# Performance work log

Measured on AMD Instinct MI355X. Metric: run time of the kernel, lower is better.

The kernel has to match this reference:

```python
import jax, jax.numpy as jnp
import numpy as np

B, S, M, D, H, F, E, K = 4, 1024, 1024, 1024, 16, 4096, 4, 2
DH = D // H
LB_COEF = 0.01
LN_EPS = 1e-5


def setup_inputs() -> dict:
    key = jax.random.key(0)
    ks = jax.random.split(key, 16)
    w = lambda k, shape: jax.random.normal(k, shape, jnp.float32) * 0.02
    return {
        "x": jax.random.normal(ks[0], (B, S, D), jnp.float32),
        "memory": jax.random.normal(ks[1], (B, M, D), jnp.float32),
        "sWq": w(ks[2], (D, D)), "sWk": w(ks[3], (D, D)),
        "sWv": w(ks[4], (D, D)), "sWo": w(ks[5], (D, D)),
        "cWq": w(ks[6], (D, D)), "cWk": w(ks[7], (D, D)),
        "cWv": w(ks[8], (D, D)), "cWo": w(ks[9], (D, D)),
        "Wg": w(ks[10], (E, D)),
        "W1": w(ks[11], (E, F, D)), "b1": jnp.zeros((E, F), jnp.float32),
        "W2": w(ks[12], (E, D, F)), "b2": jnp.zeros((E, D), jnp.float32),
        "ln1_g": jnp.ones((D,), jnp.float32), "ln1_b": jnp.zeros((D,), jnp.float32),
        "ln2_g": jnp.ones((D,), jnp.float32), "ln2_b": jnp.zeros((D,), jnp.float32),
        "ln3_g": jnp.ones((D,), jnp.float32), "ln3_b": jnp.zeros((D,), jnp.float32),
    }


def _ln(x, g, b):
    m = x.mean(-1, keepdims=True)
    v = ((x - m) ** 2).mean(-1, keepdims=True)
    return (x - m) * jax.lax.rsqrt(v + LN_EPS) * g + b


def _mha(q_in, k_in, v_in, Wq, Wk, Wv, Wo):
    # nn.Linear(bias=False): y = x @ W.T; split into heads [b, h, s, dh]
    def split(t):
        b, s, _ = t.shape
        return t.reshape(b, s, H, DH).transpose(0, 2, 1, 3)
    Q = split(q_in @ Wq.T)
    Kh = split(k_in @ Wk.T)
    V = split(v_in @ Wv.T)
    scores = jnp.einsum('bhqd,bhkd->bhqk', Q, Kh) / jnp.sqrt(jnp.float32(DH))
    attn = jax.nn.softmax(scores, axis=-1)  # dropout is identity in eval
    out = jnp.einsum('bhqk,bhkd->bhqd', attn, V)
    b, _, s, _ = out.shape
    out = out.transpose(0, 2, 1, 3).reshape(b, s, D)
    return out @ Wo.T


def _moe(h, Wg, W1, b1, W2, b2):
    gate_logits = h @ Wg.T                      # [B, S, E]
    gate_probs = jax.nn.softmax(gate_logits, -1)
    topk_logits, topk_idx = jax.lax.top_k(gate_logits, K)
    topk_w = jax.nn.softmax(topk_logits, -1)    # [B, S, K]
    # dense all-experts FFN (faithful to source): [B, S, E, F] hidden
    hid = jax.nn.gelu(jnp.einsum('bsd,efd->bsef', h, W1) + b1, approximate=False)
    eo = jnp.einsum('bsef,edf->bsed', hid, W2) + b2   # [B, S, E, D]
    sel = jnp.take_along_axis(eo, topk_idx[..., None], axis=2)  # [B, S, K, D]
    out = (sel * topk_w[..., None]).sum(axis=2)
    one_hot = jax.nn.one_hot(topk_idx, E, dtype=gate_probs.dtype)  # [B, S, K, E]
    load = one_hot.sum(axis=2).mean(axis=(0, 1))   # [E]
    imp = gate_probs.mean(axis=(0, 1))             # [E]
    aux = LB_COEF * (E * jnp.sum(load * imp))
    return out, aux


def reference(x, memory, sWq, sWk, sWv, sWo, cWq, cWk, cWv, cWo,
              Wg, W1, b1, W2, b2,
              ln1_g, ln1_b, ln2_g, ln2_b, ln3_g, ln3_b):
    h = _ln(x, ln1_g, ln1_b)
    x = x + _mha(h, h, h, sWq, sWk, sWv, sWo)
    h = _ln(x, ln2_g, ln2_b)
    x = x + _mha(h, memory, memory, cWq, cWk, cWv, cWo)
    h = _ln(x, ln3_g, ln3_b)
    ffn_out, aux = _moe(h, Wg, W1, b1, W2, b2)
    return (x + ffn_out, aux)
```

## Files before the change

kernel.cpp:

```cpp
#include <hip/hip_runtime.h>
#include <math.h>
#include <stdint.h>

typedef unsigned short u16;
typedef _Float16 f16;
typedef __attribute__((ext_vector_type(8))) _Float16 f16x8;
typedef __attribute__((ext_vector_type(8))) short s16x8;
typedef __attribute__((ext_vector_type(4))) float f32x4;
typedef __attribute__((ext_vector_type(4))) unsigned short u16x4;

#define DEV static __device__ __forceinline__

#define MFMA16(a, b, c) __builtin_amdgcn_mfma_f32_16x16x32_f16((a), (b), (c), 0, 0, 0)

DEV void split2(float v, u16& hi, u16& lo) {
  f16 h = (f16)v;
  f16 l = (f16)(v - (float)h);
  hi = __builtin_bit_cast(u16, h);
  lo = __builtin_bit_cast(u16, l);
}
DEV u16 f2h(float v) { f16 h = (f16)v; return __builtin_bit_cast(u16, h); }
DEV float h2f(u16 u) { f16 h = __builtin_bit_cast(f16, u); return (float)h; }

DEV void gload16(const void* gp, const void* lp) {
  typedef const __attribute__((address_space(1))) unsigned GU;
  typedef __attribute__((address_space(3))) unsigned LU;
  GU* g = (GU*)(uintptr_t)gp;
  LU* l = (LU*)(unsigned)(uintptr_t)lp;
  __builtin_amdgcn_global_load_lds(g, l, 16, 0, 0);
}

DEV int swzP(int q) { return ((q & 3) << 4) ^ (((q >> 2) & 3) << 5); }

enum { EPI3_SPLIT = 0, EPI3_RESID = 1 };

template <int EPI>
__global__ __launch_bounds__(256, 2)
void gemm3(const u16* __restrict__ Ah, const u16* __restrict__ Al,
           const u16* __restrict__ Bh, const u16* __restrict__ Bl,
           int N, int K, int ldC,
           u16* __restrict__ outh, u16* __restrict__ outl,
           float* __restrict__ outf, const float* __restrict__ resid)
{
  __shared__ alignas(16) u16 sAh[128 * 32], sAl[128 * 32];
  __shared__ alignas(16) u16 sBh[128 * 32], sBl[128 * 32];
  const int tid = threadIdx.x;
  const int wave = tid >> 6, lane = tid & 63;
  const int wr = wave >> 1, wc = wave & 1;
  const int li = lane & 15, g = lane >> 4;
  const long row0 = (long)blockIdx.y * 128;
  const int col0 = blockIdx.x * 128;

  const int srow = lane >> 2;
  const int scol = (lane & 3) * 8;
  const long arow = (row0 + wave * 32 + srow) * (long)K + scol;
  const long brow = ((long)col0 + wave * 32 + srow) * (long)K + scol;
  const u16 *gAh = Ah + arow, *gAl = Al + arow;
  const u16 *gBh = Bh + brow, *gBl = Bl + brow;
  u16 *lAh = sAh + wave * 1024, *lAl = sAl + wave * 1024;
  u16 *lBh = sBh + wave * 1024, *lBl = sBl + wave * 1024;

  const f32x4 fz = {0.f, 0.f, 0.f, 0.f};
  f32x4 acc[4][4];
#pragma unroll
  for (int m = 0; m < 4; m++)
#pragma unroll
    for (int n = 0; n < 4; n++) acc[m][n] = fz;

  const int aoff = (wr * 64 + li) * 32 + g * 8;
  const int boff = (wc * 64 + li) * 32 + g * 8;

  for (int k0 = 0; k0 < K; k0 += 32) {
    gload16(gAh + k0, lAh); gload16(gAh + k0 + (long)16 * K, lAh + 512);
    gload16(gAl + k0, lAl); gload16(gAl + k0 + (long)16 * K, lAl + 512);
    gload16(gBh + k0, lBh); gload16(gBh + k0 + (long)16 * K, lBh + 512);
    gload16(gBl + k0, lBl); gload16(gBl + k0 + (long)16 * K, lBl + 512);
    __syncthreads();
    f16x8 ah[4], al4[4], bh[4], bl4[4];
#pragma unroll
    for (int m = 0; m < 4; m++) {
      ah[m] = *(const f16x8*)(sAh + aoff + m * 512);
      al4[m] = *(const f16x8*)(sAl + aoff + m * 512);
    }
#pragma unroll
    for (int n = 0; n < 4; n++) {
      bh[n] = *(const f16x8*)(sBh + boff + n * 512);
      bl4[n] = *(const f16x8*)(sBl + boff + n * 512);
    }
#pragma unroll
    for (int m = 0; m < 4; m++)
#pragma unroll
      for (int n = 0; n < 4; n++) {
        f32x4 t = acc[m][n];
        t = MFMA16(al4[m], bh[n], t);
        t = MFMA16(ah[m], bl4[n], t);
        t = MFMA16(ah[m], bh[n], t);
        acc[m][n] = t;
      }
    __syncthreads();
  }

#pragma unroll
  for (int m = 0; m < 4; m++)
#pragma unroll
    for (int n = 0; n < 4; n++) {
      const int col = col0 + wc * 64 + n * 16 + li;
#pragma unroll
      for (int r = 0; r < 4; r++) {
        const long row = row0 + wr * 64 + m * 16 + g * 4 + r;
        const long idx = row * ldC + col;
        const float v = acc[m][n][r];
        if constexpr (EPI == EPI3_SPLIT) {
          u16 hi, lo; split2(v, hi, lo);
          outh[idx] = hi; outl[idx] = lo;
        } else {
          outf[idx] = resid[idx] + v;
        }
      }
    }
}

__global__ __launch_bounds__(256)
void vtrans(const u16* __restrict__ Vh, const u16* __restrict__ Vl,
            u16* __restrict__ Th, u16* __restrict__ Tl)
{
  __shared__ u16 t0[64][80];
  __shared__ u16 t1[64][80];
  const int kb = blockIdx.x, h = blockIdx.y, b = blockIdx.z;
  const int tid = threadIdx.x;
  const int r = tid >> 2;
  const int c = tid & 3;
  const long srow = ((long)b * 1024 + kb * 64 + r) * 3072 + h * 64;
  s16x8 a0 = *(const s16x8*)(Vh + srow + c * 8);
  s16x8 a1 = *(const s16x8*)(Vh + srow + c * 8 + 32);
  s16x8 b0 = *(const s16x8*)(Vl + srow + c * 8);
  s16x8 b1 = *(const s16x8*)(Vl + srow + c * 8 + 32);
#pragma unroll
  for (int j = 0; j < 8; j++) {
    t0[c * 8 + j][r]      = (u16)(short)a0[j];
    t0[c * 8 + 32 + j][r] = (u16)(short)a1[j];
    t1[c * 8 + j][r]      = (u16)(short)b0[j];
    t1[c * 8 + 32 + j][r] = (u16)(short)b1[j];
  }
  __syncthreads();
  const int dh = tid >> 2;
  const long drow = ((long)(b * 16 + h) * 64 + dh) * 1024 + kb * 64;
  s16x8 o0, o1;
#pragma unroll
  for (int j = 0; j < 8; j++) {
    o0[j] = (short)t0[dh][c * 8 + j];
    o1[j] = (short)t0[dh][c * 8 + 32 + j];
  }
  *(s16x8*)(Th + drow + c * 8) = o0;
  *(s16x8*)(Th + drow + c * 8 + 32) = o1;
#pragma unroll
  for (int j = 0; j < 8; j++) {
    o0[j] = (short)t1[dh][c * 8 + j];
    o1[j] = (short)t1[dh][c * 8 + 32 + j];
  }
  *(s16x8*)(Tl + drow + c * 8) = o0;
  *(s16x8*)(Tl + drow + c * 8 + 32) = o1;
}

__global__ __launch_bounds__(512, 4)
void attn3(const u16* __restrict__ Qh, const u16* __restrict__ Ql,
           const u16* __restrict__ Kbh, const u16* __restrict__ Kbl,
           const u16* __restrict__ Vth, const u16* __restrict__ Vtl,
           u16* __restrict__ AOh, u16* __restrict__ AOl)
{
  __shared__ alignas(16) u16 lKh[64 * 64], lKl[64 * 64];
  __shared__ alignas(16) u16 lVh[64 * 64], lVl[64 * 64];
  __shared__ alignas(16) u16 lPh[8 * 16 * 64], lPl[8 * 16 * 64];
  const int tid = threadIdx.x;
  const int wave = tid >> 6, lane = tid & 63;
  const int li = lane & 15, g = lane >> 4;
  const int qt = blockIdx.x, h = blockIdx.y, b = blockIdx.z;
  const int bh = b * 16 + h;
  const int LD = 3072;

  const long qrow0 = (long)b * 1024 + qt * 128 + wave * 16;
  f16x8 qfh[2], qfl[2];
#pragma unroll
  for (int kk = 0; kk < 2; kk++) {
    const long qoff = (qrow0 + li) * LD + h * 64 + kk * 32 + g * 8;
    qfh[kk] = *(const f16x8*)(Qh + qoff);
    qfl[kk] = *(const f16x8*)(Ql + qoff);
  }

  const f32x4 fz = {0.f, 0.f, 0.f, 0.f};
  float m_run[4], l_run[4];
  f32x4 oacc[4];
#pragma unroll
  for (int r = 0; r < 4; r++) { m_run[r] = -INFINITY; l_run[r] = 0.f; }
#pragma unroll
  for (int d = 0; d < 4; d++) oacc[d] = fz;

  char* cKh = (char*)lKh; char* cKl = (char*)lKl;
  char* cVh = (char*)lVh; char* cVl = (char*)lVl;
  char* cPh = (char*)lPh + wave * 2048;
  char* cPl = (char*)lPl + wave * 2048;

  const int kr = tid >> 3;
  const int kce = (tid & 7) * 8;
  const u16* kbase_h = Kbh + ((long)b * 1024 + kr) * LD + h * 64 + kce;
  const u16* kbase_l = Kbl + ((long)b * 1024 + kr) * LD + h * 64 + kce;
  const u16* vbase_h = Vth + ((long)bh * 64 + kr) * 1024 + kce;
  const u16* vbase_l = Vtl + ((long)bh * 64 + kr) * 1024 + kce;
  const int sdst = kr * 128 + ((kce * 2) ^ ((kr & 7) << 4));

  s16x8 rkh, rkl, rvh, rvl;
#define LOADT(t)                                                   \
  {                                                                \
    const long ko = (long)(t) * 64 * LD;                           \
    const int vo = (t) * 64;                                       \
    rkh = *(const s16x8*)(kbase_h + ko);                           \
    rkl = *(const s16x8*)(kbase_l + ko);                           \
    rvh = *(const s16x8*)(vbase_h + vo);                           \
    rvl = *(const s16x8*)(vbase_l + vo);                           \
  }

  LOADT(0);

  for (int t = 0; t < 16; ++t) {
    __syncthreads();
    *(s16x8*)(cKh + sdst) = rkh;
    *(s16x8*)(cKl + sdst) = rkl;
    *(s16x8*)(cVh + sdst) = rvh;
    *(s16x8*)(cVl + sdst) = rvl;
    if (t < 15) LOADT(t + 1);
    __syncthreads();

    f32x4 s[4];
#pragma unroll
    for (int cb = 0; cb < 4; cb++) {
      f32x4 tt = fz;
      const int key = cb * 16 + li;
#pragma unroll
      for (int kk = 0; kk < 2; kk++) {
        const int off = key * 128 + (((kk * 32 + g * 8) * 2) ^ ((key & 7) << 4));
        f16x8 fh = *(const f16x8*)(cKh + off);
        f16x8 fl = *(const f16x8*)(cKl + off);
        tt = MFMA16(qfl[kk], fh, tt);
        tt = MFMA16(qfh[kk], fl, tt);
        tt = MFMA16(qfh[kk], fh, tt);
      }
      s[cb] = tt;
    }
#pragma unroll
    for (int cb = 0; cb < 4; cb++)
#pragma unroll
      for (int r = 0; r < 4; r++) s[cb][r] *= 0.125f;

#pragma unroll
    for (int r = 0; r < 4; r++) {
      float mx = fmaxf(fmaxf(s[0][r], s[1][r]), fmaxf(s[2][r], s[3][r]));
      mx = fmaxf(mx, __shfl_xor(mx, 1));
      mx = fmaxf(mx, __shfl_xor(mx, 2));
      mx = fmaxf(mx, __shfl_xor(mx, 4));
      mx = fmaxf(mx, __shfl_xor(mx, 8));
      float mnew = fmaxf(m_run[r], mx);
      float sc = __expf(m_run[r] - mnew);
      m_run[r] = mnew;
      float ls = 0.f;
#pragma unroll
      for (int cb = 0; cb < 4; cb++) {
        float p = __expf(s[cb][r] - mnew);
        s[cb][r] = p;
        ls += p;
      }
      ls += __shfl_xor(ls, 1);
      ls += __shfl_xor(ls, 2);
      ls += __shfl_xor(ls, 4);
      ls += __shfl_xor(ls, 8);
      l_run[r] = l_run[r] * sc + ls;
#pragma unroll
      for (int d = 0; d < 4; d++) oacc[d][r] *= sc;
    }

#pragma unroll
    for (int cb = 0; cb < 4; cb++)
#pragma unroll
      for (int r = 0; r < 4; r++) {
        const int q = g * 4 + r;
        const int key = cb * 16 + li;
        const int off = q * 128 + ((key * 2) ^ swzP(q));
        u16 hi, lo; split2(s[cb][r], hi, lo);
        *(u16*)(cPh + off) = hi;
        *(u16*)(cPl + off) = lo;
      }

#pragma unroll
    for (int kk = 0; kk < 2; kk++) {
      const int kbyte = (kk * 32 + g * 8) * 2;
      const int poff = li * 128 + (kbyte ^ swzP(li));
      f16x8 pfh = *(const f16x8*)(cPh + poff);
      f16x8 pfl = *(const f16x8*)(cPl + poff);
#pragma unroll
      for (int d = 0; d < 4; d++) {
        const int dh = d * 16 + li;
        const int voff = dh * 128 + (kbyte ^ ((dh & 7) << 4));
        f16x8 vfh = *(const f16x8*)(cVh + voff);
        f16x8 vfl = *(const f16x8*)(cVl + voff);
        f32x4 tacc = oacc[d];
        tacc = MFMA16(pfl, vfh, tacc);
        tacc = MFMA16(pfh, vfl, tacc);
        tacc = MFMA16(pfh, vfh, tacc);
        oacc[d] = tacc;
      }
    }
  }
#undef LOADT

#pragma unroll
  for (int d = 0; d < 4; d++)
#pragma unroll
    for (int r = 0; r < 4; r++) {
      const long row = qrow0 + g * 4 + r;
      const int col = h * 64 + d * 16 + li;
      u16 hi, lo; split2(oacc[d][r] / l_run[r], hi, lo);
      AOh[row * 1024 + col] = hi;
      AOl[row * 1024 + col] = lo;
    }
}

template <bool GATE>
__global__ __launch_bounds__(256)
void ln_kernel(const float* __restrict__ x, const float* __restrict__ gam,
               const float* __restrict__ bet, u16* __restrict__ hh,
               u16* __restrict__ hl,
               const float* __restrict__ Wg, float* __restrict__ glog)
{
  const int row = blockIdx.x;
  const int tid = threadIdx.x;
  const int wave = tid >> 6, lane = tid & 63;
  const float* xr = x + (long)row * 1024;
  float4 v = *(const float4*)(xr + tid * 4);
  float s = v.x + v.y + v.z + v.w;
  float s2 = v.x * v.x + v.y * v.y + v.z * v.z + v.w * v.w;
#pragma unroll
  for (int m = 1; m < 64; m <<= 1) { s += __shfl_xor(s, m); s2 += __shfl_xor(s2, m); }
  __shared__ float red1[4], red2[4];
  if (lane == 0) { red1[wave] = s; red2[wave] = s2; }
  __syncthreads();
  float S = red1[0] + red1[1] + red1[2] + red1[3];
  float S2 = red2[0] + red2[1] + red2[2] + red2[3];
  float mean = S * (1.f / 1024.f);
  float var = S2 * (1.f / 1024.f) - mean * mean;
  float rstd = 1.f / sqrtf(var + 1e-5f);
  const int c = tid * 4;
  float hv[4];
  hv[0] = (v.x - mean) * rstd * gam[c + 0] + bet[c + 0];
  hv[1] = (v.y - mean) * rstd * gam[c + 1] + bet[c + 1];
  hv[2] = (v.z - mean) * rstd * gam[c + 2] + bet[c + 2];
  hv[3] = (v.w - mean) * rstd * gam[c + 3] + bet[c + 3];
  u16x4 oh, ol;
#pragma unroll
  for (int j = 0; j < 4; j++) {
    u16 hi, lo; split2(hv[j], hi, lo);
    oh[j] = hi; ol[j] = lo;
  }
  *(u16x4*)(hh + (long)row * 1024 + c) = oh;
  *(u16x4*)(hl + (long)row * 1024 + c) = ol;

  if constexpr (GATE) {
    float pe[4];
#pragma unroll
    for (int e = 0; e < 4; e++) {
      const float* wr_ = Wg + e * 1024 + c;
      pe[e] = hv[0] * wr_[0] + hv[1] * wr_[1] + hv[2] * wr_[2] + hv[3] * wr_[3];
    }
#pragma unroll
    for (int e = 0; e < 4; e++)
#pragma unroll
      for (int m = 1; m < 64; m <<= 1) pe[e] += __shfl_xor(pe[e], m);
    __shared__ float gred[4][4];
    if (lane == 0) {
#pragma unroll
      for (int e = 0; e < 4; e++) gred[wave][e] = pe[e];
    }
    __syncthreads();
    if (tid < 4)
      glog[(long)row * 4 + tid] = gred[0][tid] + gred[1][tid] + gred[2][tid] + gred[3][tid];
  }
}

__global__ __launch_bounds__(256)
void route_kernel(const float* __restrict__ glog,
                  int* __restrict__ tlist, float* __restrict__ wrow,
                  int4* __restrict__ meta, float2* __restrict__ wts,
                  int* __restrict__ scanMeta, float* __restrict__ outAux)
{
  const int tid = threadIdx.x;
  const int lane = tid & 63, wave = tid >> 6;
  __shared__ int scn[4][256];
  __shared__ int sTot[4];
  __shared__ int sBase[4];
  __shared__ float sred[4][8];

  for (int r = tid; r < 8704; r += 256) { tlist[r] = 0; wrow[r] = 0.f; }

  int myCnt[4] = {0, 0, 0, 0};
  float imp[4] = {0.f, 0.f, 0.f, 0.f}, ld[4] = {0.f, 0.f, 0.f, 0.f};
  unsigned char e1s[16], e2s[16];
  float w1s[16], w2s[16];
#pragma unroll 1
  for (int j = 0; j < 16; j++) {
    const int t = tid * 16 + j;
    float l[4];
#pragma unroll
    for (int e = 0; e < 4; e++) l[e] = glog[t * 4 + e];
    int e1 = 0; float bv = l[0];
#pragma unroll
    for (int e = 1; e < 4; e++) if (l[e] > bv) { bv = l[e]; e1 = e; }
    int e2 = -1; float bv2 = -INFINITY;
#pragma unroll
    for (int e = 0; e < 4; e++) if (e != e1 && l[e] > bv2) { bv2 = l[e]; e2 = e; }
    float wq = expf(bv2 - bv);
    float w1 = 1.f / (1.f + wq), w2 = wq / (1.f + wq);
    float ps = 0.f, pv[4];
#pragma unroll
    for (int e = 0; e < 4; e++) { pv[e] = expf(l[e] - bv); ps += pv[e]; }
    float inv = 1.f / ps;
#pragma unroll
    for (int e = 0; e < 4; e++) imp[e] += pv[e] * inv;
    ld[e1] += 1.f; ld[e2] += 1.f;
    myCnt[e1]++; myCnt[e2]++;
    e1s[j] = (unsigned char)e1; e2s[j] = (unsigned char)e2;
    w1s[j] = w1; w2s[j] = w2;
  }
#pragma unroll
  for (int e = 0; e < 4; e++) scn[e][tid] = myCnt[e];
  __syncthreads();

  if (wave < 4) {
    int carry = 0;
    for (int seg = 0; seg < 4; seg++) {
      int v = scn[wave][seg * 64 + lane];
      const int orig = v;
#pragma unroll
      for (int d = 1; d < 64; d <<= 1) { int o = __shfl_up(v, d); if (lane >= d) v += o; }
      scn[wave][seg * 64 + lane] = carry + v - orig;
      carry += __shfl(v, 63);
    }
    if (lane == 0) sTot[wave] = carry;
  }
  __syncthreads();

  if (tid == 0) {
    int base = 0;
    for (int e = 0; e < 4; e++) {
      const int c = sTot[e];
      const int cap = (c + 127) & ~127;
      sBase[e] = base;
      const int t0 = base >> 7, t1 = (base + cap) >> 7;
      for (int i = t0; i < t1; i++) scanMeta[1 + i] = e;
      base += cap;
    }
    scanMeta[0] = base >> 7;
  }
  __syncthreads();

  int off[4];
#pragma unroll
  for (int e = 0; e < 4; e++) off[e] = sBase[e] + scn[e][tid];
#pragma unroll 1
  for (int j = 0; j < 16; j++) {
    const int t = tid * 16 + j;
    const int e1 = e1s[j], e2 = e2s[j];
    const int p1 = off[e1]++;
    const int p2 = off[e2]++;
    tlist[p1] = t; wrow[p1] = w1s[j];
    tlist[p2] = t; wrow[p2] = w2s[j];
    int4 m; m.x = p1; m.y = p2; m.z = e1; m.w = e2;
    meta[t] = m;
    float2 w; w.x = w1s[j]; w.y = w2s[j];
    wts[t] = w;
  }

#pragma unroll
  for (int e = 0; e < 4; e++) {
#pragma unroll
    for (int d = 1; d < 64; d <<= 1) {
      imp[e] += __shfl_xor(imp[e], d);
      ld[e] += __shfl_xor(ld[e], d);
    }
  }
  if (lane == 0) {
#pragma unroll
    for (int e = 0; e < 4; e++) { sred[wave][e] = imp[e]; sred[wave][4 + e] = ld[e]; }
  }
  __syncthreads();
  if (tid == 0) {
    float a = 0.f;
    for (int e = 0; e < 4; e++) {
      float im = sred[0][e] + sred[1][e] + sred[2][e] + sred[3][e];
      float lo = sred[0][4 + e] + sred[1][4 + e] + sred[2][4 + e] + sred[3][4 + e];
      a += (lo * (1.f / 4096.f)) * (im * (1.f / 4096.f));
    }
    outAux[0] = 0.01f * 4.f * a;
  }
}

__global__ __launch_bounds__(256, 2)
void gemm_up(const u16* __restrict__ A, const u16* __restrict__ w1h,
             const float* __restrict__ b1, const int* __restrict__ tlist,
             const float* __restrict__ wrow, const int* __restrict__ scanMeta,
             u16* __restrict__ hid)
{
  if ((int)blockIdx.y >= scanMeta[0]) return;
  const int e = scanMeta[1 + blockIdx.y];
  __shared__ alignas(16) u16 lA[128 * 32];
  __shared__ alignas(16) u16 lB[128 * 32];
  const int tid = threadIdx.x;
  const int wave = tid >> 6, lane = tid & 63;
  const int wr = wave >> 1, wc = wave & 1;
  const int li = lane & 15, g = lane >> 4;
  const int row0 = blockIdx.y * 128;
  const int col0 = blockIdx.x * 128;

  const int srow = lane >> 2;
  const int scol = (lane & 3) * 8;
  const int r1 = row0 + wave * 32 + srow;
  const long t1 = tlist[r1], t2 = tlist[r1 + 16];
  const u16* gA1 = A + t1 * 1024 + scol;
  const u16* gA2 = A + t2 * 1024 + scol;
  const u16* gB = w1h + (size_t)e * 4194304 +
                  ((size_t)(col0 + wave * 32 + srow)) * 1024 + scol;
  u16* lAw = lA + wave * 1024;
  u16* lBw = lB + wave * 1024;

  const f32x4 fz = {0.f, 0.f, 0.f, 0.f};
  f32x4 acc[4][4];
#pragma unroll
  for (int m = 0; m < 4; m++)
#pragma unroll
    for (int n = 0; n < 4; n++) acc[m][n] = fz;

  const int aoff = (wr * 64 + li) * 32 + g * 8;
  const int boff = (wc * 64 + li) * 32 + g * 8;

  for (int k0 = 0; k0 < 1024; k0 += 32) {
    gload16(gA1 + k0, lAw);
    gload16(gA2 + k0, lAw + 512);
    gload16(gB + k0, lBw);
    gload16(gB + k0 + 16 * 1024, lBw + 512);
    __syncthreads();
    f16x8 af[4], bfr[4];
#pragma unroll
    for (int m = 0; m < 4; m++) af[m] = *(const f16x8*)(lA + aoff + m * 512);
#pragma unroll
    for (int n = 0; n < 4; n++) bfr[n] = *(const f16x8*)(lB + boff + n * 512);
#pragma unroll
    for (int m = 0; m < 4; m++)
#pragma unroll
      for (int n = 0; n < 4; n++)
        acc[m][n] = MFMA16(af[m], bfr[n], acc[m][n]);
    __syncthreads();
  }

#pragma unroll
  for (int m = 0; m < 4; m++)
#pragma unroll
    for (int n = 0; n < 4; n++) {
      const int col = col0 + wc * 64 + n * 16 + li;
#pragma unroll
      for (int r = 0; r < 4; r++) {
        const int row = row0 + wr * 64 + m * 16 + g * 4 + r;
        const float coef = wrow[row];
        float tv = acc[m][n][r] + b1[e * 4096 + col];
        float ge = 0.5f * tv * (1.f + erff(tv * 0.7071067811865475f));
        hid[(size_t)row * 4096 + col] = f2h(coef * ge);
      }
    }
}

__global__ __launch_bounds__(256, 2)
void gemm_down(const u16* __restrict__ hid, const u16* __restrict__ w2h,
               const int* __restrict__ scanMeta, u16* __restrict__ part)
{
  if ((int)blockIdx.y >= scanMeta[0]) return;
  const int e = scanMeta[1 + blockIdx.y];
  __shared__ alignas(16) u16 lA[128 * 32];
  __shared__ alignas(16) u16 lB[128 * 32];
  const int tid = threadIdx.x;
  const int wave = tid >> 6, lane = tid & 63;
  const int wr = wave >> 1, wc = wave & 1;
  const int li = lane & 15, g = lane >> 4;
  const int row0 = blockIdx.y * 128;
  const int col0 = blockIdx.x * 128;

  const int srow = lane >> 2;
  const int scol = (lane & 3) * 8;
  const u16* gA = hid + ((size_t)(row0 + wave * 32 + srow)) * 4096 + scol;
  const u16* gB = w2h + (size_t)e * 4194304 +
                  ((size_t)(col0 + wave * 32 + srow)) * 4096 + scol;
  u16* lAw = lA + wave * 1024;
  u16* lBw = lB + wave * 1024;

  const f32x4 fz = {0.f, 0.f, 0.f, 0.f};
  f32x4 acc[4][4];
#pragma unroll
  for (int m = 0; m < 4; m++)
#pragma unroll
    for (int n = 0; n < 4; n++) acc[m][n] = fz;

  const int aoff = (wr * 64 + li) * 32 + g * 8;
  const int boff = (wc * 64 + li) * 32 + g * 8;

  for (int k0 = 0; k0 < 4096; k0 += 32) {
    gload16(gA + k0, lAw);
    gload16(gA + k0 + 16 * 4096, lAw + 512);
    gload16(gB + k0, lBw);
    gload16(gB + k0 + 16 * 4096, lBw + 512);
    __syncthreads();
    f16x8 af[4], bfr[4];
#pragma unroll
    for (int m = 0; m < 4; m++) af[m] = *(const f16x8*)(lA + aoff + m * 512);
#pragma unroll
    for (int n = 0; n < 4; n++) bfr[n] = *(const f16x8*)(lB + boff + n * 512);
#pragma unroll
    for (int m = 0; m < 4; m++)
#pragma unroll
      for (int n = 0; n < 4; n++)
        acc[m][n] = MFMA16(af[m], bfr[n], acc[m][n]);
    __syncthreads();
  }

#pragma unroll
  for (int m = 0; m < 4; m++)
#pragma unroll
    for (int n = 0; n < 4; n++) {
      const int col = col0 + wc * 64 + n * 16 + li;
#pragma unroll
      for (int r = 0; r < 4; r++) {
        const int row = row0 + wr * 64 + m * 16 + g * 4 + r;
        part[(size_t)row * 1024 + col] = f2h(acc[m][n][r]);
      }
    }
}

__global__ __launch_bounds__(256)
void merge_kernel(const float* __restrict__ xw, const u16* __restrict__ part,
                  const int4* __restrict__ meta, const float2* __restrict__ wts,
                  const float* __restrict__ b2, float* __restrict__ out)
{
  const long i = ((long)blockIdx.x * 256 + threadIdx.x) * 4;
  const int row = (int)(i >> 10), col = (int)(i & 1023);
  const int4 m = meta[row];
  const float2 w = wts[row];
  float4 a = *(const float4*)(xw + i);
  u16x4 p1 = *(const u16x4*)(part + (size_t)m.x * 1024 + col);
  u16x4 p2 = *(const u16x4*)(part + (size_t)m.y * 1024 + col);
  const float* b2a = b2 + m.z * 1024 + col;
  const float* b2b = b2 + m.w * 1024 + col;
  float av[4] = {a.x, a.y, a.z, a.w};
  float4 o;
  float ov[4];
#pragma unroll
  for (int j = 0; j < 4; j++)
    ov[j] = av[j] + h2f(p1[j]) + h2f(p2[j]) + w.x * b2a[j] + w.y * b2b[j];
  o.x = ov[0]; o.y = ov[1]; o.z = ov[2]; o.w = ov[3];
  *(float4*)(out + i) = o;
}

__global__ __launch_bounds__(256)
void cvt_h(const float* __restrict__ src, u16* __restrict__ dst)
{
  const long i = ((long)blockIdx.x * 256 + threadIdx.x) * 4;
  float4 v = *(const float4*)(src + i);
  u16x4 o = {f2h(v.x), f2h(v.y), f2h(v.z), f2h(v.w)};
  *(u16x4*)(dst + i) = o;
}

__global__ __launch_bounds__(256)
void cvt_split(const float* __restrict__ src, u16* __restrict__ dh, u16* __restrict__ dl)
{
  const long i = ((long)blockIdx.x * 256 + threadIdx.x) * 4;
  float4 v = *(const float4*)(src + i);
  u16x4 oh, ol;
  float vv[4] = {v.x, v.y, v.z, v.w};
#pragma unroll
  for (int j = 0; j < 4; j++) { u16 a, b; split2(vv[j], a, b); oh[j] = a; ol[j] = b; }
  *(u16x4*)(dh + i) = oh;
  *(u16x4*)(dl + i) = ol;
}

struct Ptr8 { const float* p[8]; };

__global__ __launch_bounds__(256)
void cvt8_split(Ptr8 ps, u16* __restrict__ dh, u16* __restrict__ dl)
{
  const int w = blockIdx.y;
  const long i = ((long)blockIdx.x * 256 + threadIdx.x) * 4;
  float4 v = *(const float4*)(ps.p[w] + i);
  u16x4 oh, ol;
  float vv[4] = {v.x, v.y, v.z, v.w};
#pragma unroll
  for (int j = 0; j < 4; j++) { u16 a, b; split2(vv[j], a, b); oh[j] = a; ol[j] = b; }
  *(u16x4*)(dh + (long)w * 1048576 + i) = oh;
  *(u16x4*)(dl + (long)w * 1048576 + i) = ol;
}

extern "C" void kernel_launch(void* const* d_in, const int* in_sizes, int n_in,
                              void* d_out, int out_size, void* d_ws, size_t ws_size,
                              hipStream_t stream)
{
  const float* x    = (const float*)d_in[0];
  const float* mem  = (const float*)d_in[1];
  const float* sWq  = (const float*)d_in[2];
  const float* sWk  = (const float*)d_in[3];
  const float* sWv  = (const float*)d_in[4];
  const float* sWo  = (const float*)d_in[5];
  const float* cWq  = (const float*)d_in[6];
  const float* cWk  = (const float*)d_in[7];
  const float* cWv  = (const float*)d_in[8];
  const float* cWo  = (const float*)d_in[9];
  const float* Wg   = (const float*)d_in[10];
  const float* W1   = (const float*)d_in[11];
  const float* b1   = (const float*)d_in[12];
  const float* W2   = (const float*)d_in[13];
  const float* b2   = (const float*)d_in[14];
  const float* ln1g = (const float*)d_in[15];
  const float* ln1b = (const float*)d_in[16];
  const float* ln2g = (const float*)d_in[17];
  const float* ln2b = (const float*)d_in[18];
  const float* ln3g = (const float*)d_in[19];
  const float* ln3b = (const float*)d_in[20];
  float* out = (float*)d_out;
  (void)in_sizes; (void)n_in; (void)out_size; (void)ws_size;

  char* ws = (char*)d_ws;
  size_t off = 0;
  auto alloc = [&](size_t bytes) -> void* {
    void* p = ws + off; off += (bytes + 255) & ~(size_t)255; return p;
  };
  float* xw    = (float*)alloc((size_t)4096 * 1024 * 4);
  u16*   hh    = (u16*)  alloc((size_t)4096 * 1024 * 2);
  u16*   hl    = (u16*)  alloc((size_t)4096 * 1024 * 2);
  u16*   memh  = (u16*)  alloc((size_t)4096 * 1024 * 2);
  u16*   meml  = (u16*)  alloc((size_t)4096 * 1024 * 2);
  u16*   qkvh  = (u16*)  alloc((size_t)4096 * 3072 * 2);
  u16*   qkvl  = (u16*)  alloc((size_t)4096 * 3072 * 2);
  u16*   aoh   = (u16*)  alloc((size_t)4096 * 1024 * 2);
  u16*   aol   = (u16*)  alloc((size_t)4096 * 1024 * 2);
  u16*   aWh   = (u16*)  alloc((size_t)8 * 1024 * 1024 * 2);
  u16*   aWl   = (u16*)  alloc((size_t)8 * 1024 * 1024 * 2);
  u16*   w1h   = (u16*)  alloc((size_t)4 * 4096 * 1024 * 2);
  u16*   w2h   = (u16*)  alloc((size_t)4 * 4096 * 1024 * 2);
  float* glog  = (float*)alloc((size_t)4096 * 4 * 4);
  int*   tlist = (int*)  alloc((size_t)8704 * 4);
  float* wrow  = (float*)alloc((size_t)8704 * 4);
  int4*  meta  = (int4*) alloc((size_t)4096 * 16);
  float2* wts  = (float2*)alloc((size_t)4096 * 8);
  int*   scanM = (int*)  alloc((size_t)128 * 4);
  u16*   vth = hh;
  u16*   vtl = hl;
  u16*   hid = qkvh;
  u16*   part = (u16*)hh;

  Ptr8 p8;
  p8.p[0] = sWq; p8.p[1] = sWk; p8.p[2] = sWv; p8.p[3] = sWo;
  p8.p[4] = cWq; p8.p[5] = cWk; p8.p[6] = cWv; p8.p[7] = cWo;
  cvt8_split<<<dim3(1024, 8), 256, 0, stream>>>(p8, aWh, aWl);
  cvt_h<<<16384, 256, 0, stream>>>(W1, w1h);
  cvt_h<<<16384, 256, 0, stream>>>(W2, w2h);
  cvt_split<<<4096, 256, 0, stream>>>(mem, memh, meml);

  ln_kernel<false><<<4096, 256, 0, stream>>>(x, ln1g, ln1b, hh, hl, nullptr, nullptr);
  gemm3<EPI3_SPLIT><<<dim3(24, 32), 256, 0, stream>>>(hh, hl, aWh, aWl, 3072, 1024, 3072,
                                                      qkvh, qkvl, nullptr, nullptr);
  vtrans<<<dim3(16, 16, 4), 256, 0, stream>>>(qkvh + 2048, qkvl + 2048, vth, vtl);
  attn3<<<dim3(8, 16, 4), 512, 0, stream>>>(qkvh, qkvl, qkvh + 1024, qkvl + 1024,
                                            vth, vtl, aoh, aol);
  gemm3<EPI3_RESID><<<dim3(8, 32), 256, 0, stream>>>(aoh, aol, aWh + (size_t)3 * 1048576,
                                                     aWl + (size_t)3 * 1048576, 1024, 1024, 1024,
                                                     nullptr, nullptr, xw, x);

  ln_kernel<false><<<4096, 256, 0, stream>>>(xw, ln2g, ln2b, hh, hl, nullptr, nullptr);
  gemm3<EPI3_SPLIT><<<dim3(8, 32), 256, 0, stream>>>(hh, hl, aWh + (size_t)4 * 1048576,
                                                     aWl + (size_t)4 * 1048576, 1024, 1024, 3072,
                                                     qkvh, qkvl, nullptr, nullptr);
  gemm3<EPI3_SPLIT><<<dim3(16, 32), 256, 0, stream>>>(memh, meml, aWh + (size_t)5 * 1048576,
                                                      aWl + (size_t)5 * 1048576, 2048, 1024, 3072,
                                                      qkvh + 1024, qkvl + 1024, nullptr, nullptr);
  vtrans<<<dim3(16, 16, 4), 256, 0, stream>>>(qkvh + 2048, qkvl + 2048, vth, vtl);
  attn3<<<dim3(8, 16, 4), 512, 0, stream>>>(qkvh, qkvl, qkvh + 1024, qkvl + 1024,
                                            vth, vtl, aoh, aol);
  gemm3<EPI3_RESID><<<dim3(8, 32), 256, 0, stream>>>(aoh, aol, aWh + (size_t)7 * 1048576,
                                                     aWl + (size_t)7 * 1048576, 1024, 1024, 1024,
                                                     nullptr, nullptr, xw, xw);

  ln_kernel<true><<<4096, 256, 0, stream>>>(xw, ln3g, ln3b, hh, hl, Wg, glog);
  route_kernel<<<1, 256, 0, stream>>>(glog, tlist, wrow, meta, wts, scanM,
                                      out + (size_t)4096 * 1024);
  gemm_up<<<dim3(32, 68), 256, 0, stream>>>(hh, w1h, b1, tlist, wrow, scanM, hid);
  gemm_down<<<dim3(8, 68), 256, 0, stream>>>(hid, w2h, scanM, part);
  merge_kernel<<<4096, 256, 0, stream>>>(xw, part, meta, wts, b2, out);
}
```

Baseline: 861.3 us.

## Use 8-wave blocks in gemm3/gemm_down and remap MoE GEMM block order

The split-precision attention GEMMs and the MoE down-projection now run 512 threads (8 waves) per 128x128 tile, with each wave computing a 64x32 sub-tile. Each thread issues one global-to-LDS load per operand per k-step instead of two. Separately, gemm_up and gemm_down switch to a 1D grid whose block index is remapped so consecutive blocks are spread across row tiles in groups of 8, likely to balance expert work across XCDs and improve cache locality. The aim is more waves per CU to hide latency, at the cost of less register-level reuse per wave and more LDS reads per MFMA.

```diff
diff --git a/kernel.cpp b/kernel.cpp
--- a/kernel.cpp
+++ b/kernel.cpp
@@ -35,7 +35,7 @@
 enum { EPI3_SPLIT = 0, EPI3_RESID = 1 };
 
 template <int EPI>
-__global__ __launch_bounds__(256, 2)
+__global__ __launch_bounds__(512, 4)
 void gemm3(const u16* __restrict__ Ah, const u16* __restrict__ Al,
            const u16* __restrict__ Bh, const u16* __restrict__ Bl,
            int N, int K, int ldC,
@@ -46,51 +46,50 @@
   __shared__ alignas(16) u16 sBh[128 * 32], sBl[128 * 32];
   const int tid = threadIdx.x;
   const int wave = tid >> 6, lane = tid & 63;
-  const int wr = wave >> 1, wc = wave & 1;
+  const int wr = wave >> 2, wc = wave & 3;
   const int li = lane & 15, g = lane >> 4;
   const long row0 = (long)blockIdx.y * 128;
   const int col0 = blockIdx.x * 128;
 
-  const int srow = lane >> 2;
-  const int scol = (lane & 3) * 8;
-  const long arow = (row0 + wave * 32 + srow) * (long)K + scol;
-  const long brow = ((long)col0 + wave * 32 + srow) * (long)K + scol;
+  const int srow = tid >> 2;
+  const int scol = (tid & 3) * 8;
+  const long arow = (row0 + srow) * (long)K + scol;
+  const long brow = ((long)col0 + srow) * (long)K + scol;
   const u16 *gAh = Ah + arow, *gAl = Al + arow;
   const u16 *gBh = Bh + brow, *gBl = Bl + brow;
-  u16 *lAh = sAh + wave * 1024, *lAl = sAl + wave * 1024;
-  u16 *lBh = sBh + wave * 1024, *lBl = sBl + wave * 1024;
+  const int wbase = wave * 512;
 
   const f32x4 fz = {0.f, 0.f, 0.f, 0.f};
-  f32x4 acc[4][4];
+  f32x4 acc[4][2];
 #pragma unroll
   for (int m = 0; m < 4; m++)
 #pragma unroll
-    for (int n = 0; n < 4; n++) acc[m][n] = fz;
+    for (int n = 0; n < 2; n++) acc[m][n] = fz;
 
   const int aoff = (wr * 64 + li) * 32 + g * 8;
-  const int boff = (wc * 64 + li) * 32 + g * 8;
+  const int boff = (wc * 32 + li) * 32 + g * 8;
 
   for (int k0 = 0; k0 < K; k0 += 32) {
-    gload16(gAh + k0, lAh); gload16(gAh + k0 + (long)16 * K, lAh + 512);
-    gload16(gAl + k0, lAl); gload16(gAl + k0 + (long)16 * K, lAl + 512);
-    gload16(gBh + k0, lBh); gload16(gBh + k0 + (long)16 * K, lBh + 512);
-    gload16(gBl + k0, lBl); gload16(gBl + k0 + (long)16 * K, lBl + 512);
+    gload16(gAh + k0, sAh + wbase);
+    gload16(gAl + k0, sAl + wbase);
+    gload16(gBh + k0, sBh + wbase);
+    gload16(gBl + k0, sBl + wbase);
     __syncthreads();
-    f16x8 ah[4], al4[4], bh[4], bl4[4];
+    f16x8 ah[4], al4[4], bh[2], bl4[2];
 #pragma unroll
     for (int m = 0; m < 4; m++) {
       ah[m] = *(const f16x8*)(sAh + aoff + m * 512);
       al4[m] = *(const f16x8*)(sAl + aoff + m * 512);
     }
 #pragma unroll
-    for (int n = 0; n < 4; n++) {
+    for (int n = 0; n < 2; n++) {
       bh[n] = *(const f16x8*)(sBh + boff + n * 512);
       bl4[n] = *(const f16x8*)(sBl + boff + n * 512);
     }
 #pragma unroll
     for (int m = 0; m < 4; m++)
 #pragma unroll
-      for (int n = 0; n < 4; n++) {
+      for (int n = 0; n < 2; n++) {
         f32x4 t = acc[m][n];
         t = MFMA16(al4[m], bh[n], t);
         t = MFMA16(ah[m], bl4[n], t);
@@ -103,8 +102,8 @@
 #pragma unroll
   for (int m = 0; m < 4; m++)
 #pragma unroll
-    for (int n = 0; n < 4; n++) {
-      const int col = col0 + wc * 64 + n * 16 + li;
+    for (int n = 0; n < 2; n++) {
+      const int col = col0 + wc * 32 + n * 16 + li;
 #pragma unroll
       for (int r = 0; r < 4; r++) {
         const long row = row0 + wr * 64 + m * 16 + g * 4 + r;
@@ -507,16 +506,19 @@
              const float* __restrict__ wrow, const int* __restrict__ scanMeta,
              u16* __restrict__ hid)
 {
-  if ((int)blockIdx.y >= scanMeta[0]) return;
-  const int e = scanMeta[1 + blockIdx.y];
+  const int L = blockIdx.x;
+  const int gg = (L & 7) * 272 + (L >> 3);
+  const int rt = gg >> 5, cc = gg & 31;
+  if (rt >= scanMeta[0]) return;
+  const int e = scanMeta[1 + rt];
   __shared__ alignas(16) u16 lA[128 * 32];
   __shared__ alignas(16) u16 lB[128 * 32];
   const int tid = threadIdx.x;
   const int wave = tid >> 6, lane = tid & 63;
   const int wr = wave >> 1, wc = wave & 1;
   const int li = lane & 15, g = lane >> 4;
-  const int row0 = blockIdx.y * 128;
-  const int col0 = blockIdx.x * 128;
+  const int row0 = rt * 128;
+  const int col0 = cc * 128;
 
   const int srow = lane >> 2;
   const int scol = (lane & 3) * 8;
@@ -574,54 +576,54 @@
     }
 }
 
-__global__ __launch_bounds__(256, 2)
+__global__ __launch_bounds__(512, 4)
 void gemm_down(const u16* __restrict__ hid, const u16* __restrict__ w2h,
                const int* __restrict__ scanMeta, u16* __restrict__ part)
 {
-  if ((int)blockIdx.y >= scanMeta[0]) return;
-  const int e = scanMeta[1 + blockIdx.y];
+  const int L = blockIdx.x;
+  const int gg = (L & 7) * 68 + (L >> 3);
+  const int rt = gg >> 3, cc = gg & 7;
+  if (rt >= scanMeta[0]) return;
+  const int e = scanMeta[1 + rt];
   __shared__ alignas(16) u16 lA[128 * 32];
   __shared__ alignas(16) u16 lB[128 * 32];
   const int tid = threadIdx.x;
   const int wave = tid >> 6, lane = tid & 63;
-  const int wr = wave >> 1, wc = wave & 1;
+  const int wr = wave >> 2, wc = wave & 3;
   const int li = lane & 15, g = lane >> 4;
-  const int row0 = blockIdx.y * 128;
-  const int col0 = blockIdx.x * 128;
-
-  const int srow = lane >> 2;
-  const int scol = (lane & 3) * 8;
-  const u16* gA = hid + ((size_t)(row0 + wave * 32 + srow)) * 4096 + scol;
+  const int row0 = rt * 128;
+  const int col0 = cc * 128;
+
+  const int srow = tid >> 2;
+  const int scol = (tid & 3) * 8;
+  const u16* gA = hid + ((size_t)(row0 + srow)) * 4096 + scol;
   const u16* gB = w2h + (size_t)e * 4194304 +
-                  ((size_t)(col0 + wave * 32 + srow)) * 4096 + scol;
-  u16* lAw = lA + wave * 1024;
-  u16* lBw = lB + wave * 1024;
+                  ((size_t)(col0 + srow)) * 4096 + scol;
+  const int wbase = wave * 512;
 
   const f32x4 fz = {0.f, 0.f, 0.f, 0.f};
-  f32x4 acc[4][4];
+  f32x4 acc[4][2];
 #pragma unroll
   for (int m = 0; m < 4; m++)
 #pragma unroll
-    for (int n = 0; n < 4; n++) acc[m][n] = fz;
+    for (int n = 0; n < 2; n++) acc[m][n] = fz;
 
   const int aoff = (wr * 64 + li) * 32 + g * 8;
-  const int boff = (wc * 64 + li) * 32 + g * 8;
+  const int boff = (wc * 32 + li) * 32 + g * 8;
 
   for (int k0 = 0; k0 < 4096; k0 += 32) {
-    gload16(gA + k0, lAw);
-    gload16(gA + k0 + 16 * 4096, lAw + 512);
-    gload16(gB + k0, lBw);
-    gload16(gB + k0 + 16 * 4096, lBw + 512);
+    gload16(gA + k0, lA + wbase);
+    gload16(gB + k0, lB + wbase);
     __syncthreads();
-    f16x8 af[4], bfr[4];
+    f16x8 af[4], bfr[2];
 #pragma unroll
     for (int m = 0; m < 4; m++) af[m] = *(const f16x8*)(lA + aoff + m * 512);
 #pragma unroll
-    for (int n = 0; n < 4; n++) bfr[n] = *(const f16x8*)(lB + boff + n * 512);
+    for (int n = 0; n < 2; n++) bfr[n] = *(const f16x8*)(lB + boff + n * 512);
 #pragma unroll
     for (int m = 0; m < 4; m++)
 #pragma unroll
-      for (int n = 0; n < 4; n++)
+      for (int n = 0; n < 2; n++)
         acc[m][n] = MFMA16(af[m], bfr[n], acc[m][n]);
     __syncthreads();
   }
@@ -629,8 +631,8 @@
 #pragma unroll
   for (int m = 0; m < 4; m++)
 #pragma unroll
-    for (int n = 0; n < 4; n++) {
-      const int col = col0 + wc * 64 + n * 16 + li;
+    for (int n = 0; n < 2; n++) {
+      const int col = col0 + wc * 32 + n * 16 + li;
 #pragma unroll
       for (int r = 0; r < 4; r++) {
         const int row = row0 + wr * 64 + m * 16 + g * 4 + r;
@@ -767,33 +769,33 @@
   cvt_split<<<4096, 256, 0, stream>>>(mem, memh, meml);
 
   ln_kernel<false><<<4096, 256, 0, stream>>>(x, ln1g, ln1b, hh, hl, nullptr, nullptr);
-  gemm3<EPI3_SPLIT><<<dim3(24, 32), 256, 0, stream>>>(hh, hl, aWh, aWl, 3072, 1024, 3072,
+  gemm3<EPI3_SPLIT><<<dim3(24, 32), 512, 0, stream>>>(hh, hl, aWh, aWl, 3072, 1024, 3072,
                                                       qkvh, qkvl, nullptr, nullptr);
   vtrans<<<dim3(16, 16, 4), 256, 0, stream>>>(qkvh + 2048, qkvl + 2048, vth, vtl);
   attn3<<<dim3(8, 16, 4), 512, 0, stream>>>(qkvh, qkvl, qkvh + 1024, qkvl + 1024,
                                             vth, vtl, aoh, aol);
-  gemm3<EPI3_RESID><<<dim3(8, 32), 256, 0, stream>>>(aoh, aol, aWh + (size_t)3 * 1048576,
+  gemm3<EPI3_RESID><<<dim3(8, 32), 512, 0, stream>>>(aoh, aol, aWh + (size_t)3 * 1048576,
                                                      aWl + (size_t)3 * 1048576, 1024, 1024, 1024,
                                                      nullptr, nullptr, xw, x);
 
   ln_kernel<false><<<4096, 256, 0, stream>>>(xw, ln2g, ln2b, hh, hl, nullptr, nullptr);
-  gemm3<EPI3_SPLIT><<<dim3(8, 32), 256, 0, stream>>>(hh, hl, aWh + (size_t)4 * 1048576,
+  gemm3<EPI3_SPLIT><<<dim3(8, 32), 512, 0, stream>>>(hh, hl, aWh + (size_t)4 * 1048576,
                                                      aWl + (size_t)4 * 1048576, 1024, 1024, 3072,
                                                      qkvh, qkvl, nullptr, nullptr);
-  gemm3<EPI3_SPLIT><<<dim3(16, 32), 256, 0, stream>>>(memh, meml, aWh + (size_t)5 * 1048576,
+  gemm3<EPI3_SPLIT><<<dim3(16, 32), 512, 0, stream>>>(memh, meml, aWh + (size_t)5 * 1048576,
                                                       aWl + (size_t)5 * 1048576, 2048, 1024, 3072,
                                                       qkvh + 1024, qkvl + 1024, nullptr, nullptr);
   vtrans<<<dim3(16, 16, 4), 256, 0, stream>>>(qkvh + 2048, qkvl + 2048, vth, vtl);
   attn3<<<dim3(8, 16, 4), 512, 0, stream>>>(qkvh, qkvl, qkvh + 1024, qkvl + 1024,
                                             vth, vtl, aoh, aol);
-  gemm3<EPI3_RESID><<<dim3(8, 32), 256, 0, stream>>>(aoh, aol, aWh + (size_t)7 * 1048576,
+  gemm3<EPI3_RESID><<<dim3(8, 32), 512, 0, stream>>>(aoh, aol, aWh + (size_t)7 * 1048576,
                                                      aWl + (size_t)7 * 1048576, 1024, 1024, 1024,
                                                      nullptr, nullptr, xw, xw);
 
   ln_kernel<true><<<4096, 256, 0, stream>>>(xw, ln3g, ln3b, hh, hl, Wg, glog);
   route_kernel<<<1, 256, 0, stream>>>(glog, tlist, wrow, meta, wts, scanM,
                                       out + (size_t)4096 * 1024);
-  gemm_up<<<dim3(32, 68), 256, 0, stream>>>(hh, w1h, b1, tlist, wrow, scanM, hid);
-  gemm_down<<<dim3(8, 68), 256, 0, stream>>>(hid, w2h, scanM, part);
+  gemm_up<<<2176, 256, 0, stream>>>(hh, w1h, b1, tlist, wrow, scanM, hid);
+  gemm_down<<<544, 512, 0, stream>>>(hid, w2h, scanM, part);
   merge_kernel<<<4096, 256, 0, stream>>>(xw, part, meta, wts, b2, out);
 }
```

Result: no change. 850.4 us (-1.3%).
